# Kernel tuning notes

Hardware: AMD Instinct MI355X
Metric: run time of the kernel (lower is better)

## Reference

```python
import jax, jax.numpy as jnp
import numpy as np

L, D, H, F, V, B, S = 4, 256, 8, 2048, 1024, 4, 1024
HD = D // H
EPS = 1e-5
PARAM_NAMES = ['enc_qkv_w','enc_qkv_b','enc_out_w','enc_out_b','enc_ff1_w','enc_ff1_b','enc_ff2_w','enc_ff2_b','enc_ln1_g','enc_ln1_b','enc_ln2_g','enc_ln2_b','dec_sa_qkv_w','dec_sa_qkv_b','dec_sa_out_w','dec_sa_out_b','dec_ca_qkv_w','dec_ca_qkv_b','dec_ca_out_w','dec_ca_out_b','dec_ff1_w','dec_ff1_b','dec_ff2_w','dec_ff2_b','dec_ln1_g','dec_ln1_b','dec_ln2_g','dec_ln2_b','dec_ln3_g','dec_ln3_b']

def _ln(x, g, b):
    m = jnp.mean(x, -1, keepdims=True)
    v = jnp.mean((x - m) ** 2, -1, keepdims=True)
    return (x - m) * jax.lax.rsqrt(v + EPS) * g + b

def _mha(q_in, kv_in, qkv_w, qkv_b, out_w, out_b, key_mask=None):
    wq, wk, wv = jnp.split(qkv_w, 3, axis=0)
    bq, bk, bv = jnp.split(qkv_b, 3, axis=0)
    q = (q_in @ wq.T + bq).reshape(q_in.shape[0], -1, H, HD)
    k = (kv_in @ wk.T + bk).reshape(kv_in.shape[0], -1, H, HD)
    v = (kv_in @ wv.T + bv).reshape(kv_in.shape[0], -1, H, HD)
    scores = jnp.einsum('bqhd,bkhd->bhqk', q, k) / np.float32(np.sqrt(HD))
    if key_mask is not None:
        scores = jnp.where(key_mask[:, None, None, :], jnp.float32(-1e9), scores)
    attn = jax.nn.softmax(scores, axis=-1)
    o = jnp.einsum('bhqk,bkhd->bqhd', attn, v).reshape(q_in.shape[0], -1, D)
    return o @ out_w.T + out_b

def _forward(x, mask, codebook, pos, p):
    h = codebook[x] + pos[:, :x.shape[1], :]  # [B,S,D]
    # --- bidirectional encoder (post-LN, ReLU FFN, torch defaults) ---
    ctx = h
    for l in range(L):
        sa = _mha(ctx, ctx, p['enc_qkv_w'][l], p['enc_qkv_b'][l], p['enc_out_w'][l], p['enc_out_b'][l], mask)
        ctx = _ln(ctx + sa, p['enc_ln1_g'][l], p['enc_ln1_b'][l])
        ff = jax.nn.relu(ctx @ p['enc_ff1_w'][l].T + p['enc_ff1_b'][l]) @ p['enc_ff2_w'][l].T + p['enc_ff2_b'][l]
        ctx = _ln(ctx + ff, p['enc_ln2_g'][l], p['enc_ln2_b'][l])
    # --- depth decoder: original loops per position with tgt len 1.
    # Self-attn over a single token == out_proj(v_proj(x)); cross-attn over the
    # shared context is independent per position, so all S positions batch exactly. ---
    d = h
    for l in range(L):
        wv = p['dec_sa_qkv_w'][l][2 * D:]
        bv = p['dec_sa_qkv_b'][l][2 * D:]
        sa = (d @ wv.T + bv) @ p['dec_sa_out_w'][l].T + p['dec_sa_out_b'][l]
        d = _ln(d + sa, p['dec_ln1_g'][l], p['dec_ln1_b'][l])
        ca = _mha(d, ctx, p['dec_ca_qkv_w'][l], p['dec_ca_qkv_b'][l], p['dec_ca_out_w'][l], p['dec_ca_out_b'][l])
        d = _ln(d + ca, p['dec_ln2_g'][l], p['dec_ln2_b'][l])
        ff = jax.nn.relu(d @ p['dec_ff1_w'][l].T + p['dec_ff1_b'][l]) @ p['dec_ff2_w'][l].T + p['dec_ff2_b'][l]
        d = _ln(d + ff, p['dec_ln3_g'][l], p['dec_ln3_b'][l])
    return d

def setup_inputs() -> dict:
    key = jax.random.key(0)
    ctr = [0]
    def nk():
        k = jax.random.fold_in(key, ctr[0]); ctr[0] += 1; return k
    def prm(shape):
        return jax.random.normal(nk(), shape, jnp.float32) * 0.02
    inp = {
        'x': jax.random.randint(nk(), (B, S), 0, V),
        'mask': jnp.zeros((B, S), bool),
        'codebook': prm((V, D)),
        'pos': prm((1, V, D)),
        'enc_qkv_w': prm((L, 3 * D, D)), 'enc_qkv_b': jnp.zeros((L, 3 * D)),
        'enc_out_w': prm((L, D, D)), 'enc_out_b': jnp.zeros((L, D)),
        'enc_ff1_w': prm((L, F, D)), 'enc_ff1_b': jnp.zeros((L, F)),
        'enc_ff2_w': prm((L, D, F)), 'enc_ff2_b': jnp.zeros((L, D)),
        'enc_ln1_g': jnp.ones((L, D)), 'enc_ln1_b': jnp.zeros((L, D)),
        'enc_ln2_g': jnp.ones((L, D)), 'enc_ln2_b': jnp.zeros((L, D)),
        'dec_sa_qkv_w': prm((L, 3 * D, D)), 'dec_sa_qkv_b': jnp.zeros((L, 3 * D)),
        'dec_sa_out_w': prm((L, D, D)), 'dec_sa_out_b': jnp.zeros((L, D)),
        'dec_ca_qkv_w': prm((L, 3 * D, D)), 'dec_ca_qkv_b': jnp.zeros((L, 3 * D)),
        'dec_ca_out_w': prm((L, D, D)), 'dec_ca_out_b': jnp.zeros((L, D)),
        'dec_ff1_w': prm((L, F, D)), 'dec_ff1_b': jnp.zeros((L, F)),
        'dec_ff2_w': prm((L, D, F)), 'dec_ff2_b': jnp.zeros((L, D)),
        'dec_ln1_g': jnp.ones((L, D)), 'dec_ln1_b': jnp.zeros((L, D)),
        'dec_ln2_g': jnp.ones((L, D)), 'dec_ln2_b': jnp.zeros((L, D)),
        'dec_ln3_g': jnp.ones((L, D)), 'dec_ln3_b': jnp.zeros((L, D)),
    }
    return inp

def reference(x, mask, codebook, pos, enc_qkv_w, enc_qkv_b, enc_out_w, enc_out_b, enc_ff1_w, enc_ff1_b, enc_ff2_w, enc_ff2_b, enc_ln1_g, enc_ln1_b, enc_ln2_g, enc_ln2_b, dec_sa_qkv_w, dec_sa_qkv_b, dec_sa_out_w, dec_sa_out_b, dec_ca_qkv_w, dec_ca_qkv_b, dec_ca_out_w, dec_ca_out_b, dec_ff1_w, dec_ff1_b, dec_ff2_w, dec_ff2_b, dec_ln1_g, dec_ln1_b, dec_ln2_g, dec_ln2_b, dec_ln3_g, dec_ln3_b):
    vals = (enc_qkv_w, enc_qkv_b, enc_out_w, enc_out_b, enc_ff1_w, enc_ff1_b, enc_ff2_w, enc_ff2_b, enc_ln1_g, enc_ln1_b, enc_ln2_g, enc_ln2_b, dec_sa_qkv_w, dec_sa_qkv_b, dec_sa_out_w, dec_sa_out_b, dec_ca_qkv_w, dec_ca_qkv_b, dec_ca_out_w, dec_ca_out_b, dec_ff1_w, dec_ff1_b, dec_ff2_w, dec_ff2_b, dec_ln1_g, dec_ln1_b, dec_ln2_g, dec_ln2_b, dec_ln3_g, dec_ln3_b)
    p = dict(zip(PARAM_NAMES, vals))
    return _forward(x, mask, codebook, pos, p)
```

## Files before the change

### kernel.cpp

```cpp
#include <hip/hip_runtime.h>

typedef unsigned short u16;
typedef unsigned int   u32;
typedef short short8 __attribute__((ext_vector_type(8)));
typedef float f32x4  __attribute__((ext_vector_type(4)));

#define DEV static __device__ __forceinline__

static constexpr int S_ = 1024;
static constexpr int D_ = 256;
static constexpr int NR = 4096;

DEV u16 f2bf(float x) {
    u32 u = __float_as_uint(x);
    return (u16)((u + 0x7FFFu + ((u >> 16) & 1u)) >> 16);
}
DEV float bf2f(u16 s) { return __uint_as_float(((u32)s) << 16); }


__global__ __launch_bounds__(256) void k_fillf(float* __restrict__ o, int n, float v) {
    int i = blockIdx.x * 256 + threadIdx.x;
    if (i < n) o[i] = v;
}

__global__ __launch_bounds__(256) void k_conv_all(
        const float* __restrict__ s0, const float* __restrict__ s1, const float* __restrict__ s2,
        const float* __restrict__ s3, const float* __restrict__ s4, const float* __restrict__ s5,
        const float* __restrict__ s6, const float* __restrict__ s7, const float* __restrict__ s8,
        const float* __restrict__ s9, u16* __restrict__ dst) {
    constexpr int c0 = 786432/4,            c1 = c0 + 262144/4,  c2 = c1 + 2097152/4,
                  c3 = c2 + 2097152/4,      c4 = c3 + 786432/4,  c5 = c4 + 262144/4,
                  c6 = c5 + 786432/4,       c7 = c6 + 262144/4,  c8 = c7 + 2097152/4,
                  c9 = c8 + 2097152/4;
    for (int i = blockIdx.x * 256 + threadIdx.x; i < c9; i += gridDim.x * 256) {
        const float* src; int base;
        if      (i < c0) { src = s0; base = 0;  }
        else if (i < c1) { src = s1; base = c0; }
        else if (i < c2) { src = s2; base = c1; }
        else if (i < c3) { src = s3; base = c2; }
        else if (i < c4) { src = s4; base = c3; }
        else if (i < c5) { src = s5; base = c4; }
        else if (i < c6) { src = s6; base = c5; }
        else if (i < c7) { src = s7; base = c6; }
        else if (i < c8) { src = s8; base = c7; }
        else             { src = s9; base = c8; }
        float4 v = ((const float4*)src)[i - base];
        ushort4 o; o.x = f2bf(v.x); o.y = f2bf(v.y); o.z = f2bf(v.z); o.w = f2bf(v.w);
        ((ushort4*)dst)[i] = o;
    }
}

__global__ __launch_bounds__(256) void k_embed(const int* __restrict__ xx,
                                               const float* __restrict__ cb,
                                               const float* __restrict__ pos,
                                               float* __restrict__ hf, u16* __restrict__ hb) {
    int wid = threadIdx.x >> 6, lane = threadIdx.x & 63;
    int row = blockIdx.x * 4 + wid;
    int sp = row & (S_ - 1);
    int tok = xx[row];
    float4 c = ((const float4*)(cb + (size_t)tok * D_))[lane];
    float4 p = ((const float4*)(pos + (size_t)sp * D_))[lane];
    float4 s; s.x = c.x + p.x; s.y = c.y + p.y; s.z = c.z + p.z; s.w = c.w + p.w;
    ((float4*)(hf + (size_t)row * D_))[lane] = s;
    ushort4 o; o.x = f2bf(s.x); o.y = f2bf(s.y); o.z = f2bf(s.z); o.w = f2bf(s.w);
    ((ushort4*)(hb + (size_t)row * D_))[lane] = o;
}

__global__ __launch_bounds__(256) void k_addv(const unsigned char* __restrict__ mask,
                                              float* __restrict__ av, float* __restrict__ avz) {
    int i = blockIdx.x * 256 + threadIdx.x;
    if (i < NR) { av[i] = mask[i] ? -2.0e9f : 0.0f; avz[i] = 0.0f; }
}

__global__ __launch_bounds__(256) void k_ln(const float* __restrict__ x, const float* __restrict__ y,
                                            const float* __restrict__ gg, const float* __restrict__ bb,
                                            float* __restrict__ of, u16* __restrict__ ob) {
    int wid = threadIdx.x >> 6, lane = threadIdx.x & 63;
    int row = blockIdx.x * 4 + wid;
    float4 xv = ((const float4*)(x + (size_t)row * D_))[lane];
    float4 yv = ((const float4*)(y + (size_t)row * D_))[lane];
    float4 s; s.x = xv.x + yv.x; s.y = xv.y + yv.y; s.z = xv.z + yv.z; s.w = xv.w + yv.w;
    float sum = s.x + s.y + s.z + s.w;
    float sq  = s.x * s.x + s.y * s.y + s.z * s.z + s.w * s.w;
    #pragma unroll
    for (int m = 1; m < 64; m <<= 1) { sum += __shfl_xor(sum, m, 64); sq += __shfl_xor(sq, m, 64); }
    float mean = sum * (1.0f / 256.0f);
    float var  = sq * (1.0f / 256.0f) - mean * mean;
    float rs = rsqrtf(var + 1e-5f);
    float4 gv = ((const float4*)gg)[lane];
    float4 bv = ((const float4*)bb)[lane];
    float4 o;
    o.x = (s.x - mean) * rs * gv.x + bv.x;
    o.y = (s.y - mean) * rs * gv.y + bv.y;
    o.z = (s.z - mean) * rs * gv.z + bv.z;
    o.w = (s.w - mean) * rs * gv.w + bv.w;
    ((float4*)(of + (size_t)row * D_))[lane] = o;
    ushort4 ub; ub.x = f2bf(o.x); ub.y = f2bf(o.y); ub.z = f2bf(o.z); ub.w = f2bf(o.w);
    ((ushort4*)(ob + (size_t)row * D_))[lane] = ub;
}

__global__ __launch_bounds__(256) void k_ln4(const float* __restrict__ x, const float* __restrict__ yp,
                                             const float* __restrict__ gg, const float* __restrict__ bb,
                                             float* __restrict__ of, u16* __restrict__ ob) {
    int wid = threadIdx.x >> 6, lane = threadIdx.x & 63;
    int row = blockIdx.x * 4 + wid;
    float4 xv = ((const float4*)(x + (size_t)row * D_))[lane];
    float4 s = xv;
    #pragma unroll
    for (int kz = 0; kz < 4; kz++) {
        float4 yv = ((const float4*)(yp + (size_t)kz * NR * D_ + (size_t)row * D_))[lane];
        s.x += yv.x; s.y += yv.y; s.z += yv.z; s.w += yv.w;
    }
    float sum = s.x + s.y + s.z + s.w;
    float sq  = s.x * s.x + s.y * s.y + s.z * s.z + s.w * s.w;
    #pragma unroll
    for (int m = 1; m < 64; m <<= 1) { sum += __shfl_xor(sum, m, 64); sq += __shfl_xor(sq, m, 64); }
    float mean = sum * (1.0f / 256.0f);
    float var  = sq * (1.0f / 256.0f) - mean * mean;
    float rs = rsqrtf(var + 1e-5f);
    float4 gv = ((const float4*)gg)[lane];
    float4 bv = ((const float4*)bb)[lane];
    float4 o;
    o.x = (s.x - mean) * rs * gv.x + bv.x;
    o.y = (s.y - mean) * rs * gv.y + bv.y;
    o.z = (s.z - mean) * rs * gv.z + bv.z;
    o.w = (s.w - mean) * rs * gv.w + bv.w;
    ((float4*)(of + (size_t)row * D_))[lane] = o;
    ushort4 ub; ub.x = f2bf(o.x); ub.y = f2bf(o.y); ub.z = f2bf(o.z); ub.w = f2bf(o.w);
    ((ushort4*)(ob + (size_t)row * D_))[lane] = ub;
}


template <int BM, int BN, bool RELU, bool OBF16>
__global__ __launch_bounds__(256) void k_gemm(const u16* __restrict__ A, const u16* __restrict__ Bw,
                                              const float* __restrict__ bias,
                                              float* __restrict__ Cf, u16* __restrict__ Cb,
                                              int Nn, int Kk) {
    constexpr int FM = BM / 32, FN = BN / 32;
    constexpr int LDA = 72;
    __shared__ __align__(16) u16 As[BM * LDA];
    __shared__ __align__(16) u16 Bs[BN * LDA];
    int tid = threadIdx.x, w = tid >> 6, lane = tid & 63;
    int lr = lane & 15, g = lane >> 4;
    int wm = w >> 1, wn = w & 1;
    int nbn = Nn / BN;
    int bid = blockIdx.x, nwg = gridDim.x;
    if ((nwg & 7) == 0) bid = (bid & 7) * (nwg >> 3) + (bid >> 3);
    int m0 = (bid / nbn) * BM, n0 = (bid % nbn) * BN;
    int trow = tid >> 3, tcol = (tid & 7) << 3;

    f32x4 acc[FM][FN] = {};

    for (int kb = 0; kb < Kk; kb += 64) {
        if (kb) __syncthreads();
        #pragma unroll
        for (int r = 0; r < BM / 32; r++) {
            int row = r * 32 + trow;
            uint4 v = *(const uint4*)(A + (size_t)(m0 + row) * Kk + kb + tcol);
            *(uint4*)(As + row * LDA + tcol) = v;
        }
        #pragma unroll
        for (int r = 0; r < BN / 32; r++) {
            int row = r * 32 + trow;
            uint4 v = *(const uint4*)(Bw + (size_t)(n0 + row) * Kk + kb + tcol);
            *(uint4*)(Bs + row * LDA + tcol) = v;
        }
        __syncthreads();
        #pragma unroll
        for (int kk = 0; kk < 2; kk++) {
            short8 af[FM], bfr[FN];
            #pragma unroll
            for (int mi = 0; mi < FM; mi++)
                af[mi] = *(const short8*)(As + (wm * (BM / 2) + mi * 16 + lr) * LDA + kk * 32 + g * 8);
            #pragma unroll
            for (int ni = 0; ni < FN; ni++)
                bfr[ni] = *(const short8*)(Bs + (wn * (BN / 2) + ni * 16 + lr) * LDA + kk * 32 + g * 8);
            #pragma unroll
            for (int mi = 0; mi < FM; mi++)
                #pragma unroll
                for (int ni = 0; ni < FN; ni++)
                    acc[mi][ni] = __builtin_amdgcn_mfma_f32_16x16x32_bf16(af[mi], bfr[ni], acc[mi][ni], 0, 0, 0);
        }
    }

    #pragma unroll
    for (int ni = 0; ni < FN; ni++) {
        int col = n0 + wn * (BN / 2) + ni * 16 + lr;
        float bi = bias[col];
        #pragma unroll
        for (int mi = 0; mi < FM; mi++) {
            #pragma unroll
            for (int jj = 0; jj < 4; jj++) {
                int row = m0 + wm * (BM / 2) + mi * 16 + g * 4 + jj;
                float v = acc[mi][ni][jj] + bi;
                if (RELU) v = fmaxf(v, 0.0f);
                if (OBF16) Cb[(size_t)row * Nn + col] = f2bf(v);
                else       Cf[(size_t)row * Nn + col] = v;
            }
        }
    }
}

__global__ __launch_bounds__(256) void k_gemm_sk4(const u16* __restrict__ A, const u16* __restrict__ Bw,
                                                  const float* __restrict__ bias, float* __restrict__ Cp) {
    constexpr int LDA = 72, Nn = 256, Kk = 2048;
    __shared__ __align__(16) u16 As[64 * LDA];
    __shared__ __align__(16) u16 Bs[64 * LDA];
    int tid = threadIdx.x, w = tid >> 6, lane = tid & 63;
    int lr = lane & 15, g = lane >> 4;
    int wm = w >> 1, wn = w & 1;
    int kz = blockIdx.x >> 8;
    int mn = blockIdx.x & 255;
    mn = (mn & 7) * 32 + (mn >> 3);
    int m0 = (mn >> 2) * 64, n0 = (mn & 3) * 64;
    int kbeg = kz * 512;
    int trow = tid >> 3, tcol = (tid & 7) << 3;

    f32x4 acc[2][2] = {};

    for (int kb = kbeg; kb < kbeg + 512; kb += 64) {
        if (kb != kbeg) __syncthreads();
        #pragma unroll
        for (int r = 0; r < 2; r++) {
            int row = r * 32 + trow;
            uint4 va = *(const uint4*)(A + (size_t)(m0 + row) * Kk + kb + tcol);
            *(uint4*)(As + row * LDA + tcol) = va;
            uint4 vb = *(const uint4*)(Bw + (size_t)(n0 + row) * Kk + kb + tcol);
            *(uint4*)(Bs + row * LDA + tcol) = vb;
        }
        __syncthreads();
        #pragma unroll
        for (int kk = 0; kk < 2; kk++) {
            short8 af[2], bfr[2];
            #pragma unroll
            for (int mi = 0; mi < 2; mi++)
                af[mi] = *(const short8*)(As + (wm * 32 + mi * 16 + lr) * LDA + kk * 32 + g * 8);
            #pragma unroll
            for (int ni = 0; ni < 2; ni++)
                bfr[ni] = *(const short8*)(Bs + (wn * 32 + ni * 16 + lr) * LDA + kk * 32 + g * 8);
            #pragma unroll
            for (int mi = 0; mi < 2; mi++)
                #pragma unroll
                for (int ni = 0; ni < 2; ni++)
                    acc[mi][ni] = __builtin_amdgcn_mfma_f32_16x16x32_bf16(af[mi], bfr[ni], acc[mi][ni], 0, 0, 0);
        }
    }

    float* Cz = Cp + (size_t)kz * NR * Nn;
    #pragma unroll
    for (int ni = 0; ni < 2; ni++) {
        int col = n0 + wn * 32 + ni * 16 + lr;
        float bi = (kz == 0) ? bias[col] : 0.0f;
        #pragma unroll
        for (int mi = 0; mi < 2; mi++)
            #pragma unroll
            for (int jj = 0; jj < 4; jj++) {
                int row = m0 + wm * 32 + mi * 16 + g * 4 + jj;
                Cz[(size_t)row * Nn + col] = acc[mi][ni][jj] + bi;
            }
    }
}


__global__ __launch_bounds__(256) void k_attn(const u16* __restrict__ qp, int qs,
                                              const u16* __restrict__ kvp, int ks, int koff, int voff,
                                              const float* __restrict__ addv, u16* __restrict__ out) {
    __shared__ __align__(16) u16 Kl[128 * 32];
    __shared__ __align__(16) u16 VTl[32 * 136];
    __shared__ __align__(16) u16 Pl[4 * 16 * 136];
    __shared__ float Al[128];

    int tid = threadIdx.x, w = tid >> 6, lane = tid & 63;
    int lr = lane & 15, g = lane >> 4;
    int blk = blockIdx.x;
    blk = (blk & 7) * 64 + (blk >> 3);
    int qb = blk & 15, h = (blk >> 4) & 7, b = blk >> 7;
    int q0 = qb * 64 + w * 16;
    const float QS = 0.17677669529663687f;

    short8 qf = *(const short8*)(qp + (size_t)(b * S_ + q0 + lr) * qs + h * 32 + g * 8);

    f32x4 o0 = {0.f, 0.f, 0.f, 0.f}, o1 = {0.f, 0.f, 0.f, 0.f};
    float m_run = -3.0e38f, l_run = 0.0f;
    float sreg[8][4];
    u16* Pw = Pl + w * 16 * 136;

    int key_t = tid >> 1, dh = (tid & 1) * 16;
    const u16* kbase = kvp + (size_t)(b * S_) * ks;

    for (int kb = 0; kb < 8; kb++) {
        {
            const u16* srck = kbase + (size_t)(kb * 128 + key_t) * ks + koff + h * 32 + dh;
            uint4 a0 = *(const uint4*)srck;
            uint4 a1 = *(const uint4*)(srck + 8);
            *(uint4*)(Kl + key_t * 32 + dh) = a0;
            *(uint4*)(Kl + key_t * 32 + dh + 8) = a1;
            const u16* srcv = kbase + (size_t)(kb * 128 + key_t) * ks + voff + h * 32 + dh;
            union { uint4 v[2]; u16 s[16]; } vu;
            vu.v[0] = *(const uint4*)srcv; vu.v[1] = *(const uint4*)(srcv + 8);
            #pragma unroll
            for (int i = 0; i < 16; i++) VTl[(dh + i) * 136 + key_t] = vu.s[i];
            if (tid < 128) Al[tid] = addv[b * S_ + kb * 128 + tid];
        }
        __syncthreads();

        #pragma unroll
        for (int t = 0; t < 8; t++) {
            short8 kf = *(const short8*)(Kl + (t * 16 + lr) * 32 + g * 8);
            f32x4 z = {0.f, 0.f, 0.f, 0.f};
            f32x4 st = __builtin_amdgcn_mfma_f32_16x16x32_bf16(kf, qf, z, 0, 0, 0);
            #pragma unroll
            for (int jj = 0; jj < 4; jj++) sreg[t][jj] = st[jj] * QS + Al[t * 16 + g * 4 + jj];
        }

        float mb = -3.0e38f;
        #pragma unroll
        for (int t = 0; t < 8; t++)
            #pragma unroll
            for (int jj = 0; jj < 4; jj++) mb = fmaxf(mb, sreg[t][jj]);
        mb = fmaxf(mb, __shfl_xor(mb, 16, 64));
        mb = fmaxf(mb, __shfl_xor(mb, 32, 64));
        float mnew = fmaxf(m_run, mb);
        float sc = __expf(m_run - mnew);
        float ls = 0.f;
        #pragma unroll
        for (int t = 0; t < 8; t++)
            #pragma unroll
            for (int jj = 0; jj < 4; jj++) {
                float p = __expf(sreg[t][jj] - mnew);
                sreg[t][jj] = p; ls += p;
            }
        ls += __shfl_xor(ls, 16, 64); ls += __shfl_xor(ls, 32, 64);
        l_run = l_run * sc + ls; m_run = mnew;
        #pragma unroll
        for (int jj = 0; jj < 4; jj++) {
            float scj = __shfl(sc, 20 * g + jj, 64);
            o0[jj] *= scj; o1[jj] *= scj;
        }

        #pragma unroll
        for (int t = 0; t < 8; t++) {
            u32 u0 = (u32)f2bf(sreg[t][0]) | ((u32)f2bf(sreg[t][1]) << 16);
            u32 u1 = (u32)f2bf(sreg[t][2]) | ((u32)f2bf(sreg[t][3]) << 16);
            *(uint2*)(Pw + lr * 136 + t * 16 + g * 4) = make_uint2(u0, u1);
        }

        #pragma unroll
        for (int c = 0; c < 4; c++) {
            short8 pa = *(const short8*)(Pw + lr * 136 + c * 32 + g * 8);
            short8 v0 = *(const short8*)(VTl + lr * 136 + c * 32 + g * 8);
            short8 v1 = *(const short8*)(VTl + (16 + lr) * 136 + c * 32 + g * 8);
            o0 = __builtin_amdgcn_mfma_f32_16x16x32_bf16(pa, v0, o0, 0, 0, 0);
            o1 = __builtin_amdgcn_mfma_f32_16x16x32_bf16(pa, v1, o1, 0, 0, 0);
        }
        __syncthreads();
    }

    float li = 1.0f / l_run;
    #pragma unroll
    for (int jj = 0; jj < 4; jj++) {
        float lij = __shfl(li, 20 * g + jj, 64);
        int r = q0 + g * 4 + jj;
        u16* op = out + (size_t)(b * S_ + r) * 256 + h * 32;
        op[lr]      = f2bf(o0[jj] * lij);
        op[16 + lr] = f2bf(o1[jj] * lij);
    }
}


extern "C" void kernel_launch(void* const* d_in, const int* in_sizes, int n_in,
                              void* d_out, int out_size, void* d_ws, size_t ws_size,
                              hipStream_t stream) {
    const int* x                = (const int*)d_in[0];
    const unsigned char* mask   = (const unsigned char*)d_in[1];
    const float* codebook       = (const float*)d_in[2];
    const float* pos            = (const float*)d_in[3];
    const float* enc_qkv_w = (const float*)d_in[4];  const float* enc_qkv_b = (const float*)d_in[5];
    const float* enc_out_w = (const float*)d_in[6];  const float* enc_out_b = (const float*)d_in[7];
    const float* enc_ff1_w = (const float*)d_in[8];  const float* enc_ff1_b = (const float*)d_in[9];
    const float* enc_ff2_w = (const float*)d_in[10]; const float* enc_ff2_b = (const float*)d_in[11];
    const float* enc_ln1_g = (const float*)d_in[12]; const float* enc_ln1_b = (const float*)d_in[13];
    const float* enc_ln2_g = (const float*)d_in[14]; const float* enc_ln2_b = (const float*)d_in[15];
    const float* dec_sa_qkv_w = (const float*)d_in[16]; const float* dec_sa_qkv_b = (const float*)d_in[17];
    const float* dec_sa_out_w = (const float*)d_in[18]; const float* dec_sa_out_b = (const float*)d_in[19];
    const float* dec_ca_qkv_w = (const float*)d_in[20]; const float* dec_ca_qkv_b = (const float*)d_in[21];
    const float* dec_ca_out_w = (const float*)d_in[22]; const float* dec_ca_out_b = (const float*)d_in[23];
    const float* dec_ff1_w = (const float*)d_in[24]; const float* dec_ff1_b = (const float*)d_in[25];
    const float* dec_ff2_w = (const float*)d_in[26]; const float* dec_ff2_b = (const float*)d_in[27];
    const float* dec_ln1_g = (const float*)d_in[28]; const float* dec_ln1_b = (const float*)d_in[29];
    const float* dec_ln2_g = (const float*)d_in[30]; const float* dec_ln2_b = (const float*)d_in[31];
    const float* dec_ln3_g = (const float*)d_in[32]; const float* dec_ln3_b = (const float*)d_in[33];

    char* ws = (char*)d_ws; size_t off = 0;
    auto alloc = [&](size_t b) { char* p = ws + off; off += (b + 255) & ~(size_t)255; return p; };

    u16* w_eqkv  = (u16*)alloc((size_t)786432 * 2);
    u16* w_eout  = (u16*)alloc((size_t)262144 * 2);
    u16* w_eff1  = (u16*)alloc((size_t)2097152 * 2);
    u16* w_eff2  = (u16*)alloc((size_t)2097152 * 2);
    u16* w_dsaq  = (u16*)alloc((size_t)786432 * 2);
    u16* w_dsao  = (u16*)alloc((size_t)262144 * 2);
    u16* w_dcaq  = (u16*)alloc((size_t)786432 * 2);
    u16* w_dcao  = (u16*)alloc((size_t)262144 * 2);
    u16* w_dff1  = (u16*)alloc((size_t)2097152 * 2);
    u16* w_dff2  = (u16*)alloc((size_t)2097152 * 2);
    float* h_f   = (float*)alloc((size_t)NR * D_ * 4);
    u16*   h_b   = (u16*)  alloc((size_t)NR * D_ * 2);
    float* ctx_f = (float*)alloc((size_t)NR * D_ * 4);
    u16*   ctx_b = (u16*)  alloc((size_t)NR * D_ * 2);
    float* dd_f  = (float*)alloc((size_t)NR * D_ * 4);
    u16*   dd_b  = (u16*)  alloc((size_t)NR * D_ * 2);
    float* gem_f = (float*)alloc((size_t)NR * 256 * 4);
    float* gem_p = (float*)alloc((size_t)4 * NR * 256 * 4);
    u16*   attno = (u16*)  alloc((size_t)NR * 256 * 2);
    float* addv  = (float*)alloc((size_t)NR * 4);
    float* addvz = (float*)alloc((size_t)NR * 4);
    u16* scr = (u16*)alloc((size_t)NR * 2048 * 2);
    u16* qkv_b = scr;
    u16* ffh_b = scr;
    u16* v_b   = scr;
    u16* qca_b = scr;
    u16* kvca_b = scr + (size_t)NR * 256;
    (void)in_sizes; (void)n_in;

    if (off > ws_size) {
        k_fillf<<<(out_size + 255) / 256, 256, 0, stream>>>((float*)d_out, out_size, 1000.0f);
        return;
    }

    k_conv_all<<<2048, 256, 0, stream>>>(enc_qkv_w, enc_out_w, enc_ff1_w, enc_ff2_w,
                                         dec_sa_qkv_w, dec_sa_out_w, dec_ca_qkv_w, dec_ca_out_w,
                                         dec_ff1_w, dec_ff2_w, w_eqkv);
    k_addv<<<16, 256, 0, stream>>>(mask, addv, addvz);
    k_embed<<<1024, 256, 0, stream>>>(x, codebook, pos, h_f, h_b);

    for (int l = 0; l < 4; l++) {
        const u16* inb = l ? ctx_b : h_b;
        const float* inf = l ? ctx_f : h_f;
        k_gemm<128,128,false,true><<<192, 256, 0, stream>>>(inb, w_eqkv + (size_t)l*196608,
            enc_qkv_b + l*768, nullptr, qkv_b, 768, 256);
        k_attn<<<512, 256, 0, stream>>>(qkv_b, 768, qkv_b, 768, 256, 512, addv, attno);
        k_gemm<64,64,false,false><<<256, 256, 0, stream>>>(attno, w_eout + (size_t)l*65536,
            enc_out_b + l*256, gem_f, nullptr, 256, 256);
        k_ln<<<1024, 256, 0, stream>>>(inf, gem_f, enc_ln1_g + l*256, enc_ln1_b + l*256, ctx_f, ctx_b);
        k_gemm<128,128,true,true><<<512, 256, 0, stream>>>(ctx_b, w_eff1 + (size_t)l*524288,
            enc_ff1_b + l*2048, nullptr, ffh_b, 2048, 256);
        k_gemm_sk4<<<1024, 256, 0, stream>>>(ffh_b, w_eff2 + (size_t)l*524288,
            enc_ff2_b + l*256, gem_p);
        k_ln4<<<1024, 256, 0, stream>>>(ctx_f, gem_p, enc_ln2_g + l*256, enc_ln2_b + l*256, ctx_f, ctx_b);
    }

    for (int l = 0; l < 4; l++) {
        const u16* inb = l ? dd_b : h_b;
        const float* inf = l ? dd_f : h_f;
        k_gemm<64,64,false,true><<<256, 256, 0, stream>>>(inb, w_dsaq + (size_t)l*196608 + 131072,
            dec_sa_qkv_b + l*768 + 512, nullptr, v_b, 256, 256);
        k_gemm<64,64,false,false><<<256, 256, 0, stream>>>(v_b, w_dsao + (size_t)l*65536,
            dec_sa_out_b + l*256, gem_f, nullptr, 256, 256);
        k_ln<<<1024, 256, 0, stream>>>(inf, gem_f, dec_ln1_g + l*256, dec_ln1_b + l*256, dd_f, dd_b);
        k_gemm<64,64,false,true><<<256, 256, 0, stream>>>(dd_b, w_dcaq + (size_t)l*196608,
            dec_ca_qkv_b + l*768, nullptr, qca_b, 256, 256);
        k_gemm<64,64,false,true><<<512, 256, 0, stream>>>(ctx_b, w_dcaq + (size_t)l*196608 + 65536,
            dec_ca_qkv_b + l*768 + 256, nullptr, kvca_b, 512, 256);
        k_attn<<<512, 256, 0, stream>>>(qca_b, 256, kvca_b, 512, 0, 256, addvz, attno);
        k_gemm<64,64,false,false><<<256, 256, 0, stream>>>(attno, w_dcao + (size_t)l*65536,
            dec_ca_out_b + l*256, gem_f, nullptr, 256, 256);
        k_ln<<<1024, 256, 0, stream>>>(dd_f, gem_f, dec_ln2_g + l*256, dec_ln2_b + l*256, dd_f, dd_b);
        k_gemm<128,128,true,true><<<512, 256, 0, stream>>>(dd_b, w_dff1 + (size_t)l*524288,
            dec_ff1_b + l*2048, nullptr, ffh_b, 2048, 256);
        k_gemm_sk4<<<1024, 256, 0, stream>>>(ffh_b, w_dff2 + (size_t)l*524288,
            dec_ff2_b + l*256, gem_p);
        k_ln4<<<1024, 256, 0, stream>>>(dd_f, gem_p, dec_ln3_g + l*256, dec_ln3_b + l*256,
                                        (l == 3) ? (float*)d_out : dd_f, dd_b);
    }
}
```

Measured before the change: 646.3 us.

## Fold decoder self-attn V and out projections; double-buffer attention K/V tiles

```diff
diff --git a/kernel.cpp b/kernel.cpp
--- a/kernel.cpp
+++ b/kernel.cpp
@@ -50,10 +50,29 @@
     }
 }
 
+__global__ __launch_bounds__(256) void k_wsa(const float* __restrict__ qkvw, const float* __restrict__ qkvb,
+                                             const float* __restrict__ outw, const float* __restrict__ outb,
+                                             u16* __restrict__ wsa, float* __restrict__ bsa) {
+    int l = blockIdx.x >> 8, n = blockIdx.x & 255, t = threadIdx.x;
+    const float* wv = qkvw + (size_t)l * 196608 + 131072;
+    const float* bv = qkvb + l * 768 + 512;
+    const float* wo = outw + (size_t)l * 65536 + n * 256;
+    float acc = 0.0f, pb = 0.0f;
+    for (int j = 0; j < 256; j++) {
+        float woj = wo[j];
+        acc = fmaf(woj, wv[j * 256 + t], acc);
+        pb  = fmaf(woj, bv[j], pb);
+    }
+    wsa[(size_t)l * 65536 + n * 256 + t] = f2bf(acc);
+    if (t == 0) bsa[l * 256 + n] = pb + outb[l * 256 + n];
+}
+
 __global__ __launch_bounds__(256) void k_embed(const int* __restrict__ xx,
                                                const float* __restrict__ cb,
                                                const float* __restrict__ pos,
-                                               float* __restrict__ hf, u16* __restrict__ hb) {
+                                               const unsigned char* __restrict__ mask,
+                                               float* __restrict__ hf, u16* __restrict__ hb,
+                                               float* __restrict__ av, float* __restrict__ avz) {
     int wid = threadIdx.x >> 6, lane = threadIdx.x & 63;
     int row = blockIdx.x * 4 + wid;
     int sp = row & (S_ - 1);
@@ -64,12 +83,7 @@
     ((float4*)(hf + (size_t)row * D_))[lane] = s;
     ushort4 o; o.x = f2bf(s.x); o.y = f2bf(s.y); o.z = f2bf(s.z); o.w = f2bf(s.w);
     ((ushort4*)(hb + (size_t)row * D_))[lane] = o;
-}
-
-__global__ __launch_bounds__(256) void k_addv(const unsigned char* __restrict__ mask,
-                                              float* __restrict__ av, float* __restrict__ avz) {
-    int i = blockIdx.x * 256 + threadIdx.x;
-    if (i < NR) { av[i] = mask[i] ? -2.0e9f : 0.0f; avz[i] = 0.0f; }
+    if (lane == 0) { av[row] = mask[row] ? -2.0e9f : 0.0f; avz[row] = 0.0f; }
 }
 
 __global__ __launch_bounds__(256) void k_ln(const float* __restrict__ x, const float* __restrict__ y,
@@ -265,10 +279,10 @@
 __global__ __launch_bounds__(256) void k_attn(const u16* __restrict__ qp, int qs,
                                               const u16* __restrict__ kvp, int ks, int koff, int voff,
                                               const float* __restrict__ addv, u16* __restrict__ out) {
-    __shared__ __align__(16) u16 Kl[128 * 32];
-    __shared__ __align__(16) u16 VTl[32 * 136];
+    __shared__ __align__(16) u16 Kl[2][128 * 32];
+    __shared__ __align__(16) u16 VTl[2][32 * 136];
     __shared__ __align__(16) u16 Pl[4 * 16 * 136];
-    __shared__ float Al[128];
+    __shared__ float Al[2][128];
 
     int tid = threadIdx.x, w = tid >> 6, lane = tid & 63;
     int lr = lane & 15, g = lane >> 4;
@@ -288,30 +302,41 @@
     int key_t = tid >> 1, dh = (tid & 1) * 16;
     const u16* kbase = kvp + (size_t)(b * S_) * ks;
 
+    uint4 ka0, ka1;
+    union { uint4 v[2]; u16 s[16]; } vu;
+    float alv = 0.0f;
+    auto ldregs = [&](int kb) {
+        const u16* srck = kbase + (size_t)(kb * 128 + key_t) * ks + koff + h * 32 + dh;
+        ka0 = *(const uint4*)srck;
+        ka1 = *(const uint4*)(srck + 8);
+        const u16* srcv = kbase + (size_t)(kb * 128 + key_t) * ks + voff + h * 32 + dh;
+        vu.v[0] = *(const uint4*)srcv;
+        vu.v[1] = *(const uint4*)(srcv + 8);
+        if (tid < 128) alv = addv[b * S_ + kb * 128 + tid];
+    };
+    auto stbuf = [&](int buf) {
+        *(uint4*)(&Kl[buf][key_t * 32 + dh])     = ka0;
+        *(uint4*)(&Kl[buf][key_t * 32 + dh + 8]) = ka1;
+        #pragma unroll
+        for (int i = 0; i < 16; i++) VTl[buf][(dh + i) * 136 + key_t] = vu.s[i];
+        if (tid < 128) Al[buf][tid] = alv;
+    };
+
+    ldregs(0); stbuf(0);
+    int cur = 0;
     for (int kb = 0; kb < 8; kb++) {
-        {
-            const u16* srck = kbase + (size_t)(kb * 128 + key_t) * ks + koff + h * 32 + dh;
-            uint4 a0 = *(const uint4*)srck;
-            uint4 a1 = *(const uint4*)(srck + 8);
-            *(uint4*)(Kl + key_t * 32 + dh) = a0;
-            *(uint4*)(Kl + key_t * 32 + dh + 8) = a1;
-            const u16* srcv = kbase + (size_t)(kb * 128 + key_t) * ks + voff + h * 32 + dh;
-            union { uint4 v[2]; u16 s[16]; } vu;
-            vu.v[0] = *(const uint4*)srcv; vu.v[1] = *(const uint4*)(srcv + 8);
-            #pragma unroll
-            for (int i = 0; i < 16; i++) VTl[(dh + i) * 136 + key_t] = vu.s[i];
-            if (tid < 128) Al[tid] = addv[b * S_ + kb * 128 + tid];
-        }
         __syncthreads();
 
         #pragma unroll
         for (int t = 0; t < 8; t++) {
-            short8 kf = *(const short8*)(Kl + (t * 16 + lr) * 32 + g * 8);
+            short8 kf = *(const short8*)(&Kl[cur][(t * 16 + lr) * 32 + g * 8]);
             f32x4 z = {0.f, 0.f, 0.f, 0.f};
             f32x4 st = __builtin_amdgcn_mfma_f32_16x16x32_bf16(kf, qf, z, 0, 0, 0);
             #pragma unroll
-            for (int jj = 0; jj < 4; jj++) sreg[t][jj] = st[jj] * QS + Al[t * 16 + g * 4 + jj];
-        }
+            for (int jj = 0; jj < 4; jj++) sreg[t][jj] = st[jj] * QS + Al[cur][t * 16 + g * 4 + jj];
+        }
+
+        if (kb < 7) ldregs(kb + 1);
 
         float mb = -3.0e38f;
         #pragma unroll
@@ -348,12 +373,15 @@
         #pragma unroll
         for (int c = 0; c < 4; c++) {
             short8 pa = *(const short8*)(Pw + lr * 136 + c * 32 + g * 8);
-            short8 v0 = *(const short8*)(VTl + lr * 136 + c * 32 + g * 8);
-            short8 v1 = *(const short8*)(VTl + (16 + lr) * 136 + c * 32 + g * 8);
+            short8 v0 = *(const short8*)(&VTl[cur][lr * 136 + c * 32 + g * 8]);
+            short8 v1 = *(const short8*)(&VTl[cur][(16 + lr) * 136 + c * 32 + g * 8]);
             o0 = __builtin_amdgcn_mfma_f32_16x16x32_bf16(pa, v0, o0, 0, 0, 0);
             o1 = __builtin_amdgcn_mfma_f32_16x16x32_bf16(pa, v1, o1, 0, 0, 0);
         }
+
         __syncthreads();
+        if (kb < 7) stbuf(cur ^ 1);
+        cur ^= 1;
     }
 
     float li = 1.0f / l_run;
@@ -404,6 +432,8 @@
     u16* w_dcao  = (u16*)alloc((size_t)262144 * 2);
     u16* w_dff1  = (u16*)alloc((size_t)2097152 * 2);
     u16* w_dff2  = (u16*)alloc((size_t)2097152 * 2);
+    u16*   wsa   = (u16*)  alloc((size_t)4 * 65536 * 2);
+    float* bsa   = (float*)alloc((size_t)4 * 256 * 4);
     float* h_f   = (float*)alloc((size_t)NR * D_ * 4);
     u16*   h_b   = (u16*)  alloc((size_t)NR * D_ * 2);
     float* ctx_f = (float*)alloc((size_t)NR * D_ * 4);
@@ -418,7 +448,6 @@
     u16* scr = (u16*)alloc((size_t)NR * 2048 * 2);
     u16* qkv_b = scr;
     u16* ffh_b = scr;
-    u16* v_b   = scr;
     u16* qca_b = scr;
     u16* kvca_b = scr + (size_t)NR * 256;
     (void)in_sizes; (void)n_in;
@@ -431,8 +460,8 @@
     k_conv_all<<<2048, 256, 0, stream>>>(enc_qkv_w, enc_out_w, enc_ff1_w, enc_ff2_w,
                                          dec_sa_qkv_w, dec_sa_out_w, dec_ca_qkv_w, dec_ca_out_w,
                                          dec_ff1_w, dec_ff2_w, w_eqkv);
-    k_addv<<<16, 256, 0, stream>>>(mask, addv, addvz);
-    k_embed<<<1024, 256, 0, stream>>>(x, codebook, pos, h_f, h_b);
+    k_wsa<<<1024, 256, 0, stream>>>(dec_sa_qkv_w, dec_sa_qkv_b, dec_sa_out_w, dec_sa_out_b, wsa, bsa);
+    k_embed<<<1024, 256, 0, stream>>>(x, codebook, pos, mask, h_f, h_b, addv, addvz);
 
     for (int l = 0; l < 4; l++) {
         const u16* inb = l ? ctx_b : h_b;
@@ -453,10 +482,8 @@
     for (int l = 0; l < 4; l++) {
         const u16* inb = l ? dd_b : h_b;
         const float* inf = l ? dd_f : h_f;
-        k_gemm<64,64,false,true><<<256, 256, 0, stream>>>(inb, w_dsaq + (size_t)l*196608 + 131072,
-            dec_sa_qkv_b + l*768 + 512, nullptr, v_b, 256, 256);
-        k_gemm<64,64,false,false><<<256, 256, 0, stream>>>(v_b, w_dsao + (size_t)l*65536,
-            dec_sa_out_b + l*256, gem_f, nullptr, 256, 256);
+        k_gemm<64,64,false,false><<<256, 256, 0, stream>>>(inb, wsa + (size_t)l*65536,
+            bsa + l*256, gem_f, nullptr, 256, 256);
         k_ln<<<1024, 256, 0, stream>>>(inf, gem_f, dec_ln1_g + l*256, dec_ln1_b + l*256, dd_f, dd_b);
         k_gemm<64,64,false,true><<<256, 256, 0, stream>>>(dd_b, w_dcaq + (size_t)l*196608,
             dec_ca_qkv_b + l*768, nullptr, qca_b, 256, 256);
```

After: 620.9 us. 3.9% less time.
